# Performance work log

Measured on AMD Instinct MI355X. Metric: run time of the kernel, lower is better.

The kernel has to match this reference:

```python
import jax, jax.numpy as jnp
import numpy as np

D_MODEL = 1024
N_HEADS = 16
D_HEAD = D_MODEL // N_HEADS
BATCH = 2
SEQ = 2048


def spectral_linear(x, basis, scales):
    # (x @ U) * s @ U^T ; basis is a fixed (non-learned) square matrix
    return ((x @ basis) * scales) @ basis.T


def setup_inputs() -> dict:
    key = jax.random.key(0)
    ks = jax.random.split(key, 3)
    x = jax.random.normal(ks[0], (BATCH, SEQ, D_MODEL), dtype=jnp.float32)
    # orthonormal-ish spectral basis (random Gaussian scaled keeps values sane)
    basis = jax.random.normal(ks[1], (D_MODEL, D_MODEL), dtype=jnp.float32) / np.sqrt(D_MODEL)
    route_bias = jax.random.normal(ks[2], (N_HEADS, SEQ, SEQ), dtype=jnp.float32) * 0.02
    ones = jnp.ones((D_MODEL,), dtype=jnp.float32)
    return {
        "x": x,
        "basis": basis,
        "scale_q": ones,
        "scale_k": ones,
        "scale_v": ones,
        "scale_o": ones,
        "route_bias": route_bias,
    }


def reference(x, basis, scale_q, scale_k, scale_v, scale_o, route_bias):
    bsz, seq_len, _ = x.shape

    def split_heads(t):  # [b,s,d] -> [b,h,s,dh]
        return t.reshape(bsz, seq_len, N_HEADS, D_HEAD).transpose(0, 2, 1, 3)

    q = split_heads(spectral_linear(x, basis, scale_q))
    k = split_heads(spectral_linear(x, basis, scale_k))
    v = split_heads(spectral_linear(x, basis, scale_v))

    scores = jnp.einsum("bhqd,bhkd->bhqk", q, k) / np.sqrt(D_HEAD).astype(np.float32)
    scores = scores + route_bias[None, :, :seq_len, :seq_len]
    causal = jnp.triu(jnp.ones((seq_len, seq_len), dtype=bool), k=1)
    scores = jnp.where(causal[None, None], -jnp.inf, scores)
    attn = jax.nn.softmax(scores, axis=-1)
    out = jnp.einsum("bhqk,bhkd->bhqd", attn, v)
    out = out.transpose(0, 2, 1, 3).reshape(bsz, seq_len, D_MODEL)
    return spectral_linear(out, basis, scale_o)
```

## Files before the change

### kernel.cpp

```cpp
#include <hip/hip_runtime.h>
#include <stdint.h>

#define AS1 __attribute__((address_space(1)))
#define AS3 __attribute__((address_space(3)))

typedef __bf16 bf16x8 __attribute__((ext_vector_type(8)));
typedef float f32x4 __attribute__((ext_vector_type(4)));

#if defined(__has_builtin)
#if __has_builtin(__builtin_amdgcn_global_load_lds)
#define USE_GLL 1
#else
#define USE_GLL 0
#endif
#else
#define USE_GLL 0
#endif

static __device__ __forceinline__ unsigned short f2bf(float f) {
    union { float f; uint32_t u; } v; v.f = f;
    uint32_t u = v.u + 0x7fffu + ((v.u >> 16) & 1u);
    return (unsigned short)(u >> 16);
}

__global__ void k_f32_to_bf16(const float* __restrict__ in, unsigned short* __restrict__ out, int n) {
    int idx = (blockIdx.x * 256 + threadIdx.x) * 4;
    if (idx >= n) return;
    float4 v = *(const float4*)(in + idx);
    unsigned short r[4] = { f2bf(v.x), f2bf(v.y), f2bf(v.z), f2bf(v.w) };
    *(uint2*)(out + idx) = *(const uint2*)r;
}

__global__ void k_make_scaled(const float* __restrict__ basis,
                              const float* __restrict__ sq, const float* __restrict__ sk,
                              const float* __restrict__ sv, const float* __restrict__ so,
                              unsigned short* __restrict__ Bq, unsigned short* __restrict__ Bk,
                              unsigned short* __restrict__ Bv, unsigned short* __restrict__ Bo,
                              unsigned short* __restrict__ Ub) {
    int idx = blockIdx.x * 256 + threadIdx.x;
    int k = idx & 1023;
    float b = basis[idx];
    Bq[idx] = f2bf(b * sq[k]);
    Bk[idx] = f2bf(b * sk[k]);
    Bv[idx] = f2bf(b * sv[k]);
    Bo[idx] = f2bf(b * so[k]);
    Ub[idx] = f2bf(b);
}

__global__ void k_transpose_v(const unsigned short* __restrict__ vsb, unsigned short* __restrict__ vtb) {
    __shared__ __align__(16) unsigned short t[128 * 72];
    const int sc = blockIdx.x;
    const int bh = blockIdx.y;
    const int tid = threadIdx.x;
    #pragma unroll
    for (int rep = 0; rep < 4; ++rep) {
        int idx = rep * 256 + tid;
        int s = idx >> 3, part = idx & 7;
        *(uint4*)(t + s * 72 + part * 8) =
            *(const uint4*)(vsb + ((size_t)bh * 2048 + sc * 128 + s) * 64 + part * 8);
    }
    __syncthreads();
    #pragma unroll
    for (int rep = 0; rep < 4; ++rep) {
        int idx = rep * 256 + tid;
        int d = idx >> 4, pc = idx & 15;
        unsigned short tmp[8];
        #pragma unroll
        for (int j = 0; j < 8; ++j) tmp[j] = t[(pc * 8 + j) * 72 + d];
        *(uint4*)(vtb + ((size_t)bh * 64 + d) * 2048 + sc * 128 + pc * 8) = *(const uint4*)tmp;
    }
}

#define BK 32

__global__ __launch_bounds__(256, 2)
void k_gemm_qkv(const unsigned short* __restrict__ A,
                const unsigned short* __restrict__ B,
                unsigned short* __restrict__ qkv,
                int M, int N, int K)
{
    __shared__ __align__(16) unsigned short As[128 * BK];
    __shared__ __align__(16) unsigned short Bs[128 * BK];

    const int tid  = threadIdx.x;
    const int lane = tid & 63;
    const int w    = tid >> 6;
    const int wm   = w & 1;
    const int wn   = w >> 1;
    const int bm   = blockIdx.y;
    const int bn   = blockIdx.x;
    const int fm   = lane & 15;
    const int quad = lane >> 4;
    const int fk   = quad * 8;
    const int srow = lane >> 2;
    const int spart= lane & 3;

    f32x4 zero4 = {0.f, 0.f, 0.f, 0.f};
    f32x4 acc[4][4];
    #pragma unroll
    for (int i = 0; i < 4; ++i)
        #pragma unroll
        for (int j = 0; j < 4; ++j) acc[i][j] = zero4;

    for (int k0 = 0; k0 < K; k0 += BK) {
        #pragma unroll
        for (int t = 0; t < 2; ++t) {
            int row = w * 32 + t * 16 + srow;
            const unsigned short* ga = A + (size_t)(bm * 128 + row) * K + k0 + spart * 8;
            const unsigned short* gb = B + (size_t)(bn * 128 + row) * K + k0 + spart * 8;
#if USE_GLL
            __builtin_amdgcn_global_load_lds((const void AS1*)ga, (void AS3*)(As + w * 1024 + t * 512), 16, 0, 0);
            __builtin_amdgcn_global_load_lds((const void AS1*)gb, (void AS3*)(Bs + w * 1024 + t * 512), 16, 0, 0);
#else
            *(uint4*)(As + w * 1024 + t * 512 + lane * 8) = *(const uint4*)ga;
            *(uint4*)(Bs + w * 1024 + t * 512 + lane * 8) = *(const uint4*)gb;
#endif
        }
        __syncthreads();
        bf16x8 af[4], bfr[4];
        #pragma unroll
        for (int i = 0; i < 4; ++i) af[i] = *(const bf16x8*)(As + (wm * 64 + i * 16 + fm) * BK + fk);
        #pragma unroll
        for (int j = 0; j < 4; ++j) bfr[j] = *(const bf16x8*)(Bs + (wn * 64 + j * 16 + fm) * BK + fk);
        #pragma unroll
        for (int i = 0; i < 4; ++i)
            #pragma unroll
            for (int j = 0; j < 4; ++j)
                acc[i][j] = __builtin_amdgcn_mfma_f32_16x16x32_bf16(af[i], bfr[j], acc[i][j], 0, 0, 0);
        __syncthreads();
    }

    #pragma unroll
    for (int i = 0; i < 4; ++i)
        #pragma unroll
        for (int j = 0; j < 4; ++j)
            #pragma unroll
            for (int r = 0; r < 4; ++r) {
                int row = bm * 128 + wm * 64 + i * 16 + quad * 4 + r;
                int col = bn * 128 + wn * 64 + j * 16 + fm;
                int sec = col >> 10, cc = col & 1023;
                int bb = row >> 11, s = row & 2047;
                int hh = cc >> 6,  d = cc & 63;
                qkv[((size_t)sec << 22) + (((size_t)(bb * 16 + hh)) * 2048 + s) * 64 + d] = f2bf(acc[i][j][r]);
            }
}

template<int EPI>
__global__ __launch_bounds__(256, 2)
void k_gemm_n64(const unsigned short* __restrict__ A,
                const unsigned short* __restrict__ B,
                void* __restrict__ Cout,
                int M, int N, int K)
{
    __shared__ __align__(16) unsigned short As[128 * BK];
    __shared__ __align__(16) unsigned short Bs[64 * BK];

    const int tid  = threadIdx.x;
    const int lane = tid & 63;
    const int w    = tid >> 6;
    const int wm   = w & 1;
    const int wn   = w >> 1;
    const int bm   = blockIdx.y;
    const int bn   = blockIdx.x;
    const int fm   = lane & 15;
    const int quad = lane >> 4;
    const int fk   = quad * 8;
    const int srow = lane >> 2;
    const int spart= lane & 3;

    f32x4 zero4 = {0.f, 0.f, 0.f, 0.f};
    f32x4 acc[4][2];
    #pragma unroll
    for (int i = 0; i < 4; ++i)
        #pragma unroll
        for (int j = 0; j < 2; ++j) acc[i][j] = zero4;

    for (int k0 = 0; k0 < K; k0 += BK) {
        #pragma unroll
        for (int t = 0; t < 2; ++t) {
            int row = w * 32 + t * 16 + srow;
            const unsigned short* ga = A + (size_t)(bm * 128 + row) * K + k0 + spart * 8;
#if USE_GLL
            __builtin_amdgcn_global_load_lds((const void AS1*)ga, (void AS3*)(As + w * 1024 + t * 512), 16, 0, 0);
#else
            *(uint4*)(As + w * 1024 + t * 512 + lane * 8) = *(const uint4*)ga;
#endif
        }
        {
            const unsigned short* gb = B + (size_t)(bn * 64 + w * 16 + srow) * K + k0 + spart * 8;
#if USE_GLL
            __builtin_amdgcn_global_load_lds((const void AS1*)gb, (void AS3*)(Bs + w * 512), 16, 0, 0);
#else
            *(uint4*)(Bs + w * 512 + lane * 8) = *(const uint4*)gb;
#endif
        }
        __syncthreads();
        bf16x8 af[4], bfr[2];
        #pragma unroll
        for (int i = 0; i < 4; ++i) af[i] = *(const bf16x8*)(As + (wm * 64 + i * 16 + fm) * BK + fk);
        #pragma unroll
        for (int j = 0; j < 2; ++j) bfr[j] = *(const bf16x8*)(Bs + (wn * 32 + j * 16 + fm) * BK + fk);
        #pragma unroll
        for (int i = 0; i < 4; ++i)
            #pragma unroll
            for (int j = 0; j < 2; ++j)
                acc[i][j] = __builtin_amdgcn_mfma_f32_16x16x32_bf16(af[i], bfr[j], acc[i][j], 0, 0, 0);
        __syncthreads();
    }

    #pragma unroll
    for (int i = 0; i < 4; ++i)
        #pragma unroll
        for (int j = 0; j < 2; ++j)
            #pragma unroll
            for (int r = 0; r < 4; ++r) {
                int row = bm * 128 + wm * 64 + i * 16 + quad * 4 + r;
                int col = bn * 64 + wn * 32 + j * 16 + fm;
                if (EPI == 0) ((unsigned short*)Cout)[(size_t)row * N + col] = f2bf(acc[i][j][r]);
                else          ((float*)Cout)[(size_t)row * N + col] = acc[i][j][r];
            }
}

__global__ __launch_bounds__(256, 4)
void k_attn(const unsigned short* __restrict__ qs, const unsigned short* __restrict__ ks,
            const unsigned short* __restrict__ vt, const float* __restrict__ bias,
            unsigned short* __restrict__ out)
{
    const int qt = blockIdx.x;
    const int bh = blockIdx.y;
    const int h  = bh & 15;
    const int b  = bh >> 4;
    const size_t rowbase = (size_t)bh * 2048;

    const int tid  = threadIdx.x;
    const int lane = tid & 63;
    const int w    = tid >> 6;
    const int fm   = lane & 15;
    const int quad = lane >> 4;
    const int fk   = quad * 8;

    __shared__ __align__(16) unsigned short Ks[64 * 72];
    __shared__ __align__(16) unsigned short Vt[64 * 72];
    __shared__ __align__(16) unsigned short Ps[4][16 * 72];

    const int q0 = qt * 64 + w * 16;

    bf16x8 qf[2];
    #pragma unroll
    for (int c = 0; c < 2; ++c)
        qf[c] = *(const bf16x8*)(qs + (rowbase + q0 + fm) * 64 + c * 32 + fk);

    f32x4 zero4 = {0.f, 0.f, 0.f, 0.f};
    f32x4 oacc[4];
    float lsum[4];
    #pragma unroll
    for (int jd = 0; jd < 4; ++jd) oacc[jd] = zero4;
    #pragma unroll
    for (int r = 0; r < 4; ++r) lsum[r] = 0.f;

    const int nkt = qt + 1;
    for (int kt = 0; kt < nkt; ++kt) {
        float bb[4][4];
        #pragma unroll
        for (int jn = 0; jn < 4; ++jn)
            #pragma unroll
            for (int r = 0; r < 4; ++r)
                bb[jn][r] = bias[((size_t)h * 2048 + q0 + quad * 4 + r) * 2048
                                 + kt * 64 + jn * 16 + fm];

        #pragma unroll
        for (int rep = 0; rep < 2; ++rep) {
            int idx  = rep * 256 + tid;
            int row  = idx >> 3;
            int part = idx & 7;
            *(uint4*)(Ks + row * 72 + part * 8) =
                *(const uint4*)(ks + (rowbase + kt * 64 + row) * 64 + part * 8);
            *(uint4*)(Vt + row * 72 + part * 8) =
                *(const uint4*)(vt + ((size_t)bh * 64 + row) * 2048 + kt * 64 + part * 8);
        }
        __syncthreads();

        f32x4 sacc[4];
        #pragma unroll
        for (int jn = 0; jn < 4; ++jn) sacc[jn] = zero4;
        bf16x8 kb[4][2];
        #pragma unroll
        for (int jn = 0; jn < 4; ++jn)
            #pragma unroll
            for (int c = 0; c < 2; ++c)
                kb[jn][c] = *(const bf16x8*)(Ks + (jn * 16 + fm) * 72 + c * 32 + fk);
        #pragma unroll
        for (int jn = 0; jn < 4; ++jn)
            #pragma unroll
            for (int c = 0; c < 2; ++c)
                sacc[jn] = __builtin_amdgcn_mfma_f32_16x16x32_bf16(qf[c], kb[jn][c], sacc[jn], 0, 0, 0);

        #pragma unroll
        for (int jn = 0; jn < 4; ++jn)
            #pragma unroll
            for (int r = 0; r < 4; ++r) {
                int row = q0 + quad * 4 + r;
                int col = kt * 64 + jn * 16 + fm;
                float p = exp2f(sacc[jn][r] * 0.18033688f + bb[jn][r] * 1.44269504f);
                p = (col > row) ? 0.f : p;
                lsum[r] += p;
                Ps[w][(quad * 4 + r) * 72 + jn * 16 + fm] = f2bf(p);
            }

        bf16x8 vf[4][2], pf[2];
        #pragma unroll
        for (int jd = 0; jd < 4; ++jd)
            #pragma unroll
            for (int c = 0; c < 2; ++c)
                vf[jd][c] = *(const bf16x8*)(Vt + (jd * 16 + fm) * 72 + c * 32 + fk);
        #pragma unroll
        for (int c = 0; c < 2; ++c)
            pf[c] = *(const bf16x8*)(Ps[w] + fm * 72 + c * 32 + fk);
        #pragma unroll
        for (int jd = 0; jd < 4; ++jd)
            #pragma unroll
            for (int c = 0; c < 2; ++c)
                oacc[jd] = __builtin_amdgcn_mfma_f32_16x16x32_bf16(pf[c], vf[jd][c], oacc[jd], 0, 0, 0);

        __syncthreads();
    }

    #pragma unroll
    for (int r = 0; r < 4; ++r) {
        float l = lsum[r];
        #pragma unroll
        for (int off = 1; off < 16; off <<= 1) l += __shfl_xor(l, off, 64);
        lsum[r] = 1.f / l;
    }

    #pragma unroll
    for (int jd = 0; jd < 4; ++jd)
        #pragma unroll
        for (int r = 0; r < 4; ++r) {
            int row = q0 + quad * 4 + r;
            int d   = jd * 16 + fm;
            out[((size_t)b * 2048 + row) * 1024 + h * 64 + d] = f2bf(oacc[jd][r] * lsum[r]);
        }
}

extern "C" void kernel_launch(void* const* d_in, const int* in_sizes, int n_in,
                              void* d_out, int out_size, void* d_ws, size_t ws_size,
                              hipStream_t stream) {
    (void)in_sizes; (void)n_in; (void)out_size; (void)ws_size;
    const float* x     = (const float*)d_in[0];
    const float* basis = (const float*)d_in[1];
    const float* sq    = (const float*)d_in[2];
    const float* sk    = (const float*)d_in[3];
    const float* sv    = (const float*)d_in[4];
    const float* so    = (const float*)d_in[5];
    const float* bias  = (const float*)d_in[6];
    float* out = (float*)d_out;

    char* ws = (char*)d_ws;
    size_t off = 0;
    auto alloc = [&](size_t bytes) { void* p = ws + off; off += bytes; return p; };
    unsigned short* x_bf  = (unsigned short*)alloc((size_t)8 << 20);
    unsigned short* Acat  = (unsigned short*)alloc((size_t)8 << 20);
    unsigned short* Ub    = (unsigned short*)alloc((size_t)2 << 20);
    unsigned short* Wall  = (unsigned short*)alloc((size_t)8 << 20);
    unsigned short* qkvb  = (unsigned short*)alloc((size_t)24 << 20);
    unsigned short* vtb   = (unsigned short*)alloc((size_t)8 << 20);
    unsigned short* attno = (unsigned short*)alloc((size_t)8 << 20);

    unsigned short* Bq  = Acat;
    unsigned short* Bk  = Acat + ((size_t)1 << 20);
    unsigned short* Bv  = Acat + ((size_t)2 << 20);
    unsigned short* Bo  = Acat + ((size_t)3 << 20);
    unsigned short* qsb = qkvb;
    unsigned short* ksb = qkvb + ((size_t)1 << 22);
    unsigned short* vsb = qkvb + ((size_t)2 << 22);
    unsigned short* Wo  = Wall + (size_t)3 * 1024 * 1024;

    k_f32_to_bf16<<<4096, 256, 0, stream>>>(x, x_bf, 4096 * 1024);
    k_make_scaled<<<4096, 256, 0, stream>>>(basis, sq, sk, sv, so, Bq, Bk, Bv, Bo, Ub);

    dim3 blk(256);
    k_gemm_n64<0><<<dim3(16, 32), blk, 0, stream>>>(Acat, Ub, Wall, 4096, 1024, 1024);
    k_gemm_qkv<<<dim3(24, 32), blk, 0, stream>>>(x_bf, Wall, qkvb, 4096, 3072, 1024);
    k_transpose_v<<<dim3(16, 32), blk, 0, stream>>>(vsb, vtb);
    k_attn<<<dim3(32, 32), blk, 0, stream>>>(qsb, ksb, vtb, bias, attno);
    k_gemm_n64<2><<<dim3(16, 32), blk, 0, stream>>>(attno, Wo, out, 4096, 1024, 1024);
}
```

Before: 516.0 us.

## Enlarge attention query tile to 128 rows, reverse tile order, group heads by batch

Each wave in the attention kernel now handles 32 query rows instead of 16, so every K/V tile staged in shared memory is reused across twice as many queries. This halves the number of blocks and the total K/V global loads. Query tiles are launched in reverse order so the longest causal blocks start first, and blockIdx.y is remapped so both batches of a head sit next to each other, which may help the bias stay in cache. The cost is more registers per thread, with launch bounds relaxed from 4 to 2 blocks per CU, and fewer blocks to spread across the GPU.

```diff
diff --git a/kernel.cpp b/kernel.cpp
--- a/kernel.cpp
+++ b/kernel.cpp
@@ -221,15 +221,16 @@
             }
 }
 
-__global__ __launch_bounds__(256, 4)
+__global__ __launch_bounds__(256, 2)
 void k_attn(const unsigned short* __restrict__ qs, const unsigned short* __restrict__ ks,
             const unsigned short* __restrict__ vt, const float* __restrict__ bias,
             unsigned short* __restrict__ out)
 {
-    const int qt = blockIdx.x;
-    const int bh = blockIdx.y;
-    const int h  = bh & 15;
-    const int b  = bh >> 4;
+    const int qt = 15 - blockIdx.x;
+    const int by = blockIdx.y;
+    const int h  = by >> 1;
+    const int b  = by & 1;
+    const int bh = b * 16 + h;
     const size_t rowbase = (size_t)bh * 2048;
 
     const int tid  = threadIdx.x;
@@ -241,32 +242,39 @@
 
     __shared__ __align__(16) unsigned short Ks[64 * 72];
     __shared__ __align__(16) unsigned short Vt[64 * 72];
-    __shared__ __align__(16) unsigned short Ps[4][16 * 72];
-
-    const int q0 = qt * 64 + w * 16;
-
-    bf16x8 qf[2];
-    #pragma unroll
-    for (int c = 0; c < 2; ++c)
-        qf[c] = *(const bf16x8*)(qs + (rowbase + q0 + fm) * 64 + c * 32 + fk);
+    __shared__ __align__(16) unsigned short Ps[4][32 * 72];
+
+    const int q0 = qt * 128 + w * 32;
+
+    bf16x8 qf[2][2];
+    #pragma unroll
+    for (int g = 0; g < 2; ++g)
+        #pragma unroll
+        for (int c = 0; c < 2; ++c)
+            qf[g][c] = *(const bf16x8*)(qs + (rowbase + q0 + g * 16 + fm) * 64 + c * 32 + fk);
 
     f32x4 zero4 = {0.f, 0.f, 0.f, 0.f};
-    f32x4 oacc[4];
-    float lsum[4];
-    #pragma unroll
-    for (int jd = 0; jd < 4; ++jd) oacc[jd] = zero4;
-    #pragma unroll
-    for (int r = 0; r < 4; ++r) lsum[r] = 0.f;
-
-    const int nkt = qt + 1;
+    f32x4 oacc[2][4];
+    float lsum[2][4];
+    #pragma unroll
+    for (int g = 0; g < 2; ++g) {
+        #pragma unroll
+        for (int jd = 0; jd < 4; ++jd) oacc[g][jd] = zero4;
+        #pragma unroll
+        for (int r = 0; r < 4; ++r) lsum[g][r] = 0.f;
+    }
+
+    const int nkt = qt * 2 + 2;
     for (int kt = 0; kt < nkt; ++kt) {
-        float bb[4][4];
-        #pragma unroll
-        for (int jn = 0; jn < 4; ++jn)
-            #pragma unroll
-            for (int r = 0; r < 4; ++r)
-                bb[jn][r] = bias[((size_t)h * 2048 + q0 + quad * 4 + r) * 2048
-                                 + kt * 64 + jn * 16 + fm];
+        float bb[2][4][4];
+        #pragma unroll
+        for (int g = 0; g < 2; ++g)
+            #pragma unroll
+            for (int jn = 0; jn < 4; ++jn)
+                #pragma unroll
+                for (int r = 0; r < 4; ++r)
+                    bb[g][jn][r] = bias[((size_t)h * 2048 + q0 + g * 16 + quad * 4 + r) * 2048
+                                        + kt * 64 + jn * 16 + fm];
 
         #pragma unroll
         for (int rep = 0; rep < 2; ++rep) {
@@ -280,67 +288,81 @@
         }
         __syncthreads();
 
-        f32x4 sacc[4];
-        #pragma unroll
-        for (int jn = 0; jn < 4; ++jn) sacc[jn] = zero4;
         bf16x8 kb[4][2];
         #pragma unroll
         for (int jn = 0; jn < 4; ++jn)
             #pragma unroll
             for (int c = 0; c < 2; ++c)
                 kb[jn][c] = *(const bf16x8*)(Ks + (jn * 16 + fm) * 72 + c * 32 + fk);
-        #pragma unroll
-        for (int jn = 0; jn < 4; ++jn)
-            #pragma unroll
-            for (int c = 0; c < 2; ++c)
-                sacc[jn] = __builtin_amdgcn_mfma_f32_16x16x32_bf16(qf[c], kb[jn][c], sacc[jn], 0, 0, 0);
-
-        #pragma unroll
-        for (int jn = 0; jn < 4; ++jn)
-            #pragma unroll
-            for (int r = 0; r < 4; ++r) {
-                int row = q0 + quad * 4 + r;
-                int col = kt * 64 + jn * 16 + fm;
-                float p = exp2f(sacc[jn][r] * 0.18033688f + bb[jn][r] * 1.44269504f);
-                p = (col > row) ? 0.f : p;
-                lsum[r] += p;
-                Ps[w][(quad * 4 + r) * 72 + jn * 16 + fm] = f2bf(p);
-            }
-
-        bf16x8 vf[4][2], pf[2];
+        f32x4 sacc[2][4];
+        #pragma unroll
+        for (int g = 0; g < 2; ++g)
+            #pragma unroll
+            for (int jn = 0; jn < 4; ++jn) sacc[g][jn] = zero4;
+        #pragma unroll
+        for (int g = 0; g < 2; ++g)
+            #pragma unroll
+            for (int jn = 0; jn < 4; ++jn)
+                #pragma unroll
+                for (int c = 0; c < 2; ++c)
+                    sacc[g][jn] = __builtin_amdgcn_mfma_f32_16x16x32_bf16(qf[g][c], kb[jn][c], sacc[g][jn], 0, 0, 0);
+
+        #pragma unroll
+        for (int g = 0; g < 2; ++g)
+            #pragma unroll
+            for (int jn = 0; jn < 4; ++jn)
+                #pragma unroll
+                for (int r = 0; r < 4; ++r) {
+                    int row = q0 + g * 16 + quad * 4 + r;
+                    int col = kt * 64 + jn * 16 + fm;
+                    float p = exp2f(sacc[g][jn][r] * 0.18033688f + bb[g][jn][r] * 1.44269504f);
+                    p = (col > row) ? 0.f : p;
+                    lsum[g][r] += p;
+                    Ps[w][(g * 16 + quad * 4 + r) * 72 + jn * 16 + fm] = f2bf(p);
+                }
+
+        bf16x8 vf[4][2], pf[2][2];
         #pragma unroll
         for (int jd = 0; jd < 4; ++jd)
             #pragma unroll
             for (int c = 0; c < 2; ++c)
                 vf[jd][c] = *(const bf16x8*)(Vt + (jd * 16 + fm) * 72 + c * 32 + fk);
         #pragma unroll
-        for (int c = 0; c < 2; ++c)
-            pf[c] = *(const bf16x8*)(Ps[w] + fm * 72 + c * 32 + fk);
+        for (int g = 0; g < 2; ++g)
+            #pragma unroll
+            for (int c = 0; c < 2; ++c)
+                pf[g][c] = *(const bf16x8*)(Ps[w] + (g * 16 + fm) * 72 + c * 32 + fk);
+        #pragma unroll
+        for (int g = 0; g < 2; ++g)
+            #pragma unroll
+            for (int jd = 0; jd < 4; ++jd)
+                #pragma unroll
+                for (int c = 0; c < 2; ++c)
+                    oacc[g][jd] = __builtin_amdgcn_mfma_f32_16x16x32_bf16(pf[g][c], vf[jd][c], oacc[g][jd], 0, 0, 0);
+
+        __syncthreads();
+    }
+
+    #pragma unroll
+    for (int g = 0; g < 2; ++g)
+        #pragma unroll
+        for (int r = 0; r < 4; ++r) {
+            float l = lsum[g][r];
+            #pragma unroll
+            for (int off = 1; off < 16; off <<= 1) l += __shfl_xor(l, off, 64);
+            lsum[g][r] = 1.f / l;
+        }
+
+    #pragma unroll
+    for (int g = 0; g < 2; ++g)
         #pragma unroll
         for (int jd = 0; jd < 4; ++jd)
             #pragma unroll
-            for (int c = 0; c < 2; ++c)
-                oacc[jd] = __builtin_amdgcn_mfma_f32_16x16x32_bf16(pf[c], vf[jd][c], oacc[jd], 0, 0, 0);
-
-        __syncthreads();
-    }
-
-    #pragma unroll
-    for (int r = 0; r < 4; ++r) {
-        float l = lsum[r];
-        #pragma unroll
-        for (int off = 1; off < 16; off <<= 1) l += __shfl_xor(l, off, 64);
-        lsum[r] = 1.f / l;
-    }
-
-    #pragma unroll
-    for (int jd = 0; jd < 4; ++jd)
-        #pragma unroll
-        for (int r = 0; r < 4; ++r) {
-            int row = q0 + quad * 4 + r;
-            int d   = jd * 16 + fm;
-            out[((size_t)b * 2048 + row) * 1024 + h * 64 + d] = f2bf(oacc[jd][r] * lsum[r]);
-        }
+            for (int r = 0; r < 4; ++r) {
+                int row = q0 + g * 16 + quad * 4 + r;
+                int d   = jd * 16 + fm;
+                out[((size_t)b * 2048 + row) * 1024 + h * 64 + d] = f2bf(oacc[g][jd][r] * lsum[g][r]);
+            }
 }
 
 extern "C" void kernel_launch(void* const* d_in, const int* in_sizes, int n_in,
@@ -383,6 +405,6 @@
     k_gemm_n64<0><<<dim3(16, 32), blk, 0, stream>>>(Acat, Ub, Wall, 4096, 1024, 1024);
     k_gemm_qkv<<<dim3(24, 32), blk, 0, stream>>>(x_bf, Wall, qkvb, 4096, 3072, 1024);
     k_transpose_v<<<dim3(16, 32), blk, 0, stream>>>(vsb, vtb);
-    k_attn<<<dim3(32, 32), blk, 0, stream>>>(qsb, ksb, vtb, bias, attno);
+    k_attn<<<dim3(16, 32), blk, 0, stream>>>(qsb, ksb, vtb, bias, attno);
     k_gemm_n64<2><<<dim3(16, 32), blk, 0, stream>>>(attno, Wo, out, 4096, 1024, 1024);
 }
```

Measured after the change: 511.6 us. No clear change (-0.9%).
